# Kernel tuning notes

Measured on AMD Instinct MI355X. Metric: run time of the kernel, lower is better.

Reference implementation:

```python
import jax, jax.numpy as jnp
import numpy as np

HIDDEN = [256, 256, 256]
COND = 30
NB_STEPS = 20  # Clenshaw-Curtis quadrature order -> NB_STEPS+1 nodes


def cc_weights_steps(nb_steps):
    # Clenshaw-Curtis weights/nodes on [-1, 1] (UMNN compute_cc_weights)
    lam = np.arange(nb_steps + 1, dtype=np.float64).reshape(-1, 1)
    lam = np.cos(lam @ lam.T * np.pi / nb_steps)
    lam[:, 0] *= 0.5
    lam[:, -1] *= 0.5
    lam = lam * 2.0 / nb_steps
    W = np.arange(nb_steps + 1, dtype=np.float64).reshape(-1, 1)
    W[1::2] = 0.0
    W = 2.0 / (1.0 - W ** 2)
    W[0] = 1.0
    W[1::2] = 0.0
    cc_w = (lam.T @ W).flatten()          # [S]
    steps = np.cos(np.arange(nb_steps + 1) * np.pi / nb_steps)  # [S]
    return jnp.asarray(cc_w, jnp.float32), jnp.asarray(steps, jnp.float32)


def mlp(inp, Ws, bs):
    # IntegrandNet: Linear+ReLU chain, final layer ELU(x)+1 (strictly positive)
    y = inp
    n = len(Ws)
    for i in range(n):
        y = y @ Ws[i] + bs[i]
        y = jax.nn.relu(y) if i < n - 1 else jax.nn.elu(y) + 1.0
    return y[..., 0]


def setup_inputs() -> dict:
    key = jax.random.key(0)
    ks = jax.random.split(key, 12)
    B, D = 512, 32
    x = jax.random.normal(ks[0], (B, D), jnp.float32)
    h = jax.random.normal(ks[1], (B, D, COND), jnp.float32)
    dims = [1 + COND] + HIDDEN + [1]
    params = {}
    for i in range(len(dims) - 1):
        params[f"W{i}"] = jax.random.normal(ks[2 + 2 * i], (dims[i], dims[i + 1]), jnp.float32) / np.sqrt(dims[i]).astype(np.float32)
        params[f"b{i}"] = jnp.zeros((dims[i + 1],), jnp.float32)
    return {"x": x, "h": h, **params}


def reference(x, h, W0, b0, W1, b1, W2, b2, W3, b3):
    Ws = [W0, W1, W2, W3]
    bs = [b0, b1, b2, b3]
    B, D = x.shape
    S = NB_STEPS + 1
    cc_w, steps = cc_weights_steps(NB_STEPS)
    # x0 = 0, xT = x -> quadrature nodes X = xT * (steps + 1) / 2, shape [B, S, D]
    X = x[:, None, :] * (steps[None, :, None] + 1.0) * 0.5
    hb = jnp.broadcast_to(h[:, None, :, :], (B, S, D, COND))
    inp = jnp.concatenate([X[..., None], hb], axis=-1)  # [B, S, D, 1+COND]
    f = mlp(inp, Ws, bs)                                 # [B, S, D] positive integrand
    z_est = jnp.einsum('bsd,s->bd', f, cc_w) * x * 0.5   # integral over [0, x]
    z = z_est + h[:, :, 0]                               # add offset z0
    # second output: integrand evaluated at x (the transform's Jacobian diag)
    inp_x = jnp.concatenate([x[..., None], h], axis=-1)  # [B, D, 1+COND]
    jac = mlp(inp_x, Ws, bs)                             # [B, D]
    return z, jac
```

## Files before the change

kernel.cpp:

```cpp
#include <hip/hip_runtime.h>
#include <math.h>

#define NB        512
#define ND        32
#define NCOND     30
#define NS        21
#define NBD       (NB*ND)
#define BDPB      3
#define NBLK      ((NBD + BDPB - 1) / BDPB)

#define W0P_ELEMS (1*16*64*8)
#define W1P_ELEMS (8*16*64*8)
#define W3P_ELEMS (8*64*8)
#define WP_TOTAL  (W0P_ELEMS + 2*W1P_ELEMS + W3P_ELEMS)

typedef __bf16 bf8 __attribute__((ext_vector_type(8)));
typedef float  fx4 __attribute__((ext_vector_type(4)));
typedef unsigned short us8 __attribute__((ext_vector_type(8)));

__device__ __forceinline__ unsigned short f2bf(float f) {
  unsigned int u = __float_as_uint(f);
  u += 0x7FFFu + ((u >> 16) & 1u);
  return (unsigned short)(u >> 16);
}

__global__ void prep_pack(const float* __restrict__ W0,
                          const float* __restrict__ W1,
                          const float* __restrict__ W2,
                          const float* __restrict__ W3,
                          unsigned short* __restrict__ wp,
                          float* __restrict__ ccwbuf) {
  if (blockIdx.x == 0 && threadIdx.x < NS) {
    int tid = threadIdx.x;
    double acc = 0.0;
#pragma unroll
    for (int i = 0; i <= 20; i += 2) {
      double wi = (i == 0) ? 1.0 : 2.0 / (1.0 - (double)(i * i));
      acc += cos((double)(i * tid) * 3.141592653589793 / 20.0) * wi;
    }
    double edge = (tid == 0 || tid == 20) ? 0.5 : 1.0;
    ccwbuf[tid] = (float)(acc * 0.1 * edge);
  }
  int t = blockIdx.x * blockDim.x + threadIdx.x;
  if (t >= WP_TOTAL / 8) return;
  int base = t * 8;
  us8 out;
  if (base >= W0P_ELEMS + 2 * W1P_ELEMS) {
    int rem  = base - (W0P_ELEMS + 2 * W1P_ELEMS);
    int lane = (rem >> 3) & 63;
    int ktl  = rem >> 9;
    int k0   = ktl * 32 + (lane >> 4) * 8;
#pragma unroll
    for (int i = 0; i < 8; ++i)
      out[i] = ((lane & 15) == 0) ? f2bf(W3[k0 + i]) : (unsigned short)0;
  } else {
    const float* W; int rem, K;
    if (base < W0P_ELEMS)                  { W = W0; rem = base;                 K = 31;  }
    else if (base < W0P_ELEMS + W1P_ELEMS) { W = W1; rem = base - W0P_ELEMS;     K = 256; }
    else                                   { W = W2; rem = base - W0P_ELEMS - W1P_ELEMS; K = 256; }
    int lane = (rem >> 3) & 63;
    int ct   = (rem >> 9) & 15;
    int ktl  =  rem >> 13;
    int j  = ct * 16 + (lane & 15);
    int k0 = ktl * 32 + (lane >> 4) * 8;
#pragma unroll
    for (int i = 0; i < 8; ++i) {
      int k = k0 + i;
      out[i] = (k < K) ? f2bf(W[k * 256 + j]) : (unsigned short)0;
    }
  }
  *reinterpret_cast<us8*>(wp + base) = out;
}


#define ACC_BIAS(BIAS)                                                           \
  {                                                                              \
    float4 bq0 = *reinterpret_cast<const float4*>((BIAS) + (cgrp * 4 + 0) * 16 + khalf * 4); \
    float4 bq1 = *reinterpret_cast<const float4*>((BIAS) + (cgrp * 4 + 1) * 16 + khalf * 4); \
    float4 bq2 = *reinterpret_cast<const float4*>((BIAS) + (cgrp * 4 + 2) * 16 + khalf * 4); \
    float4 bq3 = *reinterpret_cast<const float4*>((BIAS) + (cgrp * 4 + 3) * 16 + khalf * 4); \
    _Pragma("unroll")                                                            \
    for (int rt = 0; rt < 4; ++rt) {                                             \
      acc[rt][0] = fx4{bq0.x, bq0.y, bq0.z, bq0.w};                              \
      acc[rt][1] = fx4{bq1.x, bq1.y, bq1.z, bq1.w};                              \
      acc[rt][2] = fx4{bq2.x, bq2.y, bq2.z, bq2.w};                              \
      acc[rt][3] = fx4{bq3.x, bq3.y, bq3.z, bq3.w};                              \
    }                                                                            \
  }

#define LOADW4(S0,S1,S2,S3, WB, KT)                                              \
  S0 = *reinterpret_cast<const bf8*>((WB) + (((KT) * 16 + cgrp * 4 + 0) * 64 + lane) * 8); \
  S1 = *reinterpret_cast<const bf8*>((WB) + (((KT) * 16 + cgrp * 4 + 1) * 64 + lane) * 8); \
  S2 = *reinterpret_cast<const bf8*>((WB) + (((KT) * 16 + cgrp * 4 + 2) * 64 + lane) * 8); \
  S3 = *reinterpret_cast<const bf8*>((WB) + (((KT) * 16 + cgrp * 4 + 3) * 64 + lane) * 8);

#define AOFF(M, KT) (((unsigned)((M) * 512 + (KT) * 64 + khalf * 16)) ^ ((unsigned)(((M) & 15) << 4)))

#define KSTEP(SRC, W0_,W1_,W2_,W3_, KT)                                          \
  {                                                                              \
    bf8 a0 = *reinterpret_cast<const bf8*>((SRC) + AOFF( 0 + colb, KT));         \
    bf8 a1 = *reinterpret_cast<const bf8*>((SRC) + AOFF(16 + colb, KT));         \
    bf8 a2 = *reinterpret_cast<const bf8*>((SRC) + AOFF(32 + colb, KT));         \
    bf8 a3 = *reinterpret_cast<const bf8*>((SRC) + AOFF(48 + colb, KT));         \
    __builtin_amdgcn_s_setprio(1);                                               \
    acc[0][0] = __builtin_amdgcn_mfma_f32_16x16x32_bf16(W0_, a0, acc[0][0], 0, 0, 0); \
    acc[0][1] = __builtin_amdgcn_mfma_f32_16x16x32_bf16(W1_, a0, acc[0][1], 0, 0, 0); \
    acc[0][2] = __builtin_amdgcn_mfma_f32_16x16x32_bf16(W2_, a0, acc[0][2], 0, 0, 0); \
    acc[0][3] = __builtin_amdgcn_mfma_f32_16x16x32_bf16(W3_, a0, acc[0][3], 0, 0, 0); \
    acc[1][0] = __builtin_amdgcn_mfma_f32_16x16x32_bf16(W0_, a1, acc[1][0], 0, 0, 0); \
    acc[1][1] = __builtin_amdgcn_mfma_f32_16x16x32_bf16(W1_, a1, acc[1][1], 0, 0, 0); \
    acc[1][2] = __builtin_amdgcn_mfma_f32_16x16x32_bf16(W2_, a1, acc[1][2], 0, 0, 0); \
    acc[1][3] = __builtin_amdgcn_mfma_f32_16x16x32_bf16(W3_, a1, acc[1][3], 0, 0, 0); \
    acc[2][0] = __builtin_amdgcn_mfma_f32_16x16x32_bf16(W0_, a2, acc[2][0], 0, 0, 0); \
    acc[2][1] = __builtin_amdgcn_mfma_f32_16x16x32_bf16(W1_, a2, acc[2][1], 0, 0, 0); \
    acc[2][2] = __builtin_amdgcn_mfma_f32_16x16x32_bf16(W2_, a2, acc[2][2], 0, 0, 0); \
    acc[2][3] = __builtin_amdgcn_mfma_f32_16x16x32_bf16(W3_, a2, acc[2][3], 0, 0, 0); \
    acc[3][0] = __builtin_amdgcn_mfma_f32_16x16x32_bf16(W0_, a3, acc[3][0], 0, 0, 0); \
    acc[3][1] = __builtin_amdgcn_mfma_f32_16x16x32_bf16(W1_, a3, acc[3][1], 0, 0, 0); \
    acc[3][2] = __builtin_amdgcn_mfma_f32_16x16x32_bf16(W2_, a3, acc[3][2], 0, 0, 0); \
    acc[3][3] = __builtin_amdgcn_mfma_f32_16x16x32_bf16(W3_, a3, acc[3][3], 0, 0, 0); \
    __builtin_amdgcn_s_setprio(0);                                               \
  }

#define DENSE_PIPE(SRC, WB, NWB)                                                 \
  KSTEP(SRC, wa0,wa1,wa2,wa3, 0) LOADW4(wa0,wa1,wa2,wa3, WB, 2)                  \
  KSTEP(SRC, wb0,wb1,wb2,wb3, 1) LOADW4(wb0,wb1,wb2,wb3, WB, 3)                  \
  KSTEP(SRC, wa0,wa1,wa2,wa3, 2) LOADW4(wa0,wa1,wa2,wa3, WB, 4)                  \
  KSTEP(SRC, wb0,wb1,wb2,wb3, 3) LOADW4(wb0,wb1,wb2,wb3, WB, 5)                  \
  KSTEP(SRC, wa0,wa1,wa2,wa3, 4) LOADW4(wa0,wa1,wa2,wa3, WB, 6)                  \
  KSTEP(SRC, wb0,wb1,wb2,wb3, 5) LOADW4(wb0,wb1,wb2,wb3, WB, 7)                  \
  KSTEP(SRC, wa0,wa1,wa2,wa3, 6) LOADW4(wa0,wa1,wa2,wa3, NWB, 0)                 \
  KSTEP(SRC, wb0,wb1,wb2,wb3, 7) LOADW4(wb0,wb1,wb2,wb3, NWB, 1)

#define DENSE_LAST(SRC, WB)                                                      \
  KSTEP(SRC, wa0,wa1,wa2,wa3, 0) LOADW4(wa0,wa1,wa2,wa3, WB, 2)                  \
  KSTEP(SRC, wb0,wb1,wb2,wb3, 1) LOADW4(wb0,wb1,wb2,wb3, WB, 3)                  \
  KSTEP(SRC, wa0,wa1,wa2,wa3, 2) LOADW4(wa0,wa1,wa2,wa3, WB, 4)                  \
  KSTEP(SRC, wb0,wb1,wb2,wb3, 3) LOADW4(wb0,wb1,wb2,wb3, WB, 5)                  \
  KSTEP(SRC, wa0,wa1,wa2,wa3, 4) LOADW4(wa0,wa1,wa2,wa3, WB, 6)                  \
  KSTEP(SRC, wb0,wb1,wb2,wb3, 5) LOADW4(wb0,wb1,wb2,wb3, WB, 7)                  \
  KSTEP(SRC, wa0,wa1,wa2,wa3, 6)                                                 \
  KSTEP(SRC, wb0,wb1,wb2,wb3, 7)

#define ACT_STORE(DST)                                                           \
  {                                                                              \
    _Pragma("unroll")                                                            \
    for (int rt = 0; rt < 4; ++rt) {                                             \
      int m = rt * 16 + colb;                                                    \
      unsigned int sbase = (unsigned int)(m * 512);                              \
      unsigned int swz   = (unsigned int)((m & 15) << 4);                        \
      _Pragma("unroll")                                                          \
      for (int ct = 0; ct < 4; ++ct) {                                           \
        int n0 = (cgrp * 4 + ct) * 16 + khalf * 4;                               \
        float v0 = fmaxf(acc[rt][ct][0], 0.f);                                   \
        float v1 = fmaxf(acc[rt][ct][1], 0.f);                                   \
        float v2 = fmaxf(acc[rt][ct][2], 0.f);                                   \
        float v3 = fmaxf(acc[rt][ct][3], 0.f);                                   \
        unsigned int p0, p1;                                                     \
        asm("v_cvt_pk_bf16_f32 %0, %1, %2" : "=v"(p0) : "v"(v0), "v"(v1));       \
        asm("v_cvt_pk_bf16_f32 %0, %1, %2" : "=v"(p1) : "v"(v2), "v"(v3));       \
        uint2 pk; pk.x = p0; pk.y = p1;                                          \
        *reinterpret_cast<uint2*>((DST) + ((sbase + (unsigned int)(n0 * 2)) ^ swz)) = pk; \
      }                                                                          \
    }                                                                            \
  }

__global__ __launch_bounds__(256, 2)
void mlp_kernel(const float* __restrict__ x, const float* __restrict__ h,
                const float* __restrict__ b0, const float* __restrict__ b1,
                const float* __restrict__ b2, const float* __restrict__ b3,
                const unsigned short* __restrict__ wp,
                const float* __restrict__ ccw,
                float* __restrict__ out) {
  __shared__ __align__(16) unsigned char ldsA[64 * 512];
  __shared__ __align__(16) unsigned char ldsB[64 * 512];
  __shared__ float ldsF[64];
  unsigned char* ldsIn = ldsB;

  int tid  = threadIdx.x;
  int wv   = tid >> 6;
  int lane = tid & 63;
  int cgrp = wv;
  int colb  = lane & 15;
  int khalf = lane >> 4;
  int blkbd = blockIdx.x * BDPB;

  const unsigned short* wb1p = wp + W0P_ELEMS;
  const unsigned short* wb2p = wp + W0P_ELEMS + W1P_ELEMS;
  const unsigned short* w3p  = wp + W0P_ELEMS + 2 * W1P_ELEMS;

  bf8 wa0, wa1, wa2, wa3, wb0, wb1, wb2, wb3;
  LOADW4(wa0, wa1, wa2, wa3, wp, 0);

  {
    int r = tid >> 2;
    int q = tid & 3;
    unsigned int u = (unsigned int)r / NS;
    int s = r - (int)u * NS;
    int bd = blkbd + (int)u;
    us8 au = us8{0,0,0,0,0,0,0,0};
    if (r < 63 && bd < NBD) {
      float xv = x[bd];
      float node = xv * (cosf((float)s * 0.15707963267948966f) + 1.0f) * 0.5f;
      const float* hrow = h + bd * NCOND;
#pragma unroll
      for (int i = 0; i < 8; ++i) {
        int c = q * 8 + i;
        float v;
        if (c == 0)       v = node;
        else if (c <= 30) v = hrow[c - 1];
        else              v = 0.0f;
        au[i] = f2bf(v);
      }
    }
    unsigned int off = (unsigned int)(r * 64 + q * 16) ^ (unsigned int)((r & 3) << 4);
    *reinterpret_cast<us8*>(ldsIn + off) = au;
  }
  __syncthreads();

  fx4 acc[4][4];

  {
    ACC_BIAS(b0);
#pragma unroll
    for (int rt = 0; rt < 4; ++rt) {
      int m = rt * 16 + colb;
      unsigned int off = (unsigned int)(m * 64 + khalf * 16) ^ (unsigned int)((m & 3) << 4);
      bf8 a = *reinterpret_cast<const bf8*>(ldsIn + off);
      acc[rt][0] = __builtin_amdgcn_mfma_f32_16x16x32_bf16(wa0, a, acc[rt][0], 0, 0, 0);
      acc[rt][1] = __builtin_amdgcn_mfma_f32_16x16x32_bf16(wa1, a, acc[rt][1], 0, 0, 0);
      acc[rt][2] = __builtin_amdgcn_mfma_f32_16x16x32_bf16(wa2, a, acc[rt][2], 0, 0, 0);
      acc[rt][3] = __builtin_amdgcn_mfma_f32_16x16x32_bf16(wa3, a, acc[rt][3], 0, 0, 0);
    }
    LOADW4(wa0, wa1, wa2, wa3, wb1p, 0);
    LOADW4(wb0, wb1, wb2, wb3, wb1p, 1);
    ACT_STORE(ldsA);
  }
  __syncthreads();

  ACC_BIAS(b1);
  DENSE_PIPE(ldsA, wb1p, wb2p);
  ACT_STORE(ldsB);
  __syncthreads();

  ACC_BIAS(b2);
  DENSE_LAST(ldsB, wb2p);
  ACT_STORE(ldsA);
  __syncthreads();

  {
    fx4 a3 = fx4{0.f, 0.f, 0.f, 0.f};
    int m = wv * 16 + colb;
    unsigned int abase = (unsigned int)(m * 512 + khalf * 16);
    unsigned int aswz  = (unsigned int)((m & 15) << 4);
#pragma unroll
    for (int kt = 0; kt < 8; ++kt) {
      bf8 w3f = *reinterpret_cast<const bf8*>(w3p + (kt * 64 + lane) * 8);
      bf8 a = *reinterpret_cast<const bf8*>(ldsA + ((abase + (unsigned)(kt * 64)) ^ aswz));
      a3 = __builtin_amdgcn_mfma_f32_16x16x32_bf16(w3f, a, a3, 0, 0, 0);
    }
    if (lane < 16) {
      float y = a3[0] + b3[0];
      float f = (y > 0.f) ? (y + 1.f) : expf(y);
      ldsF[wv * 16 + lane] = f;
    }
  }
  __syncthreads();

  if (tid < BDPB) {
    int bd = blkbd + tid;
    if (bd < NBD) {
      float acc2 = 0.f;
#pragma unroll
      for (int s2 = 0; s2 < NS; ++s2) acc2 += ldsF[tid * NS + s2] * ccw[s2];
      out[bd] = acc2 * x[bd] * 0.5f + h[bd * NCOND];
      out[NBD + bd] = ldsF[tid * NS];
    }
  }
}

extern "C" void kernel_launch(void* const* d_in, const int* in_sizes, int n_in,
                              void* d_out, int out_size, void* d_ws, size_t ws_size,
                              hipStream_t stream) {
  (void)in_sizes; (void)n_in; (void)out_size; (void)ws_size;
  const float* x  = (const float*)d_in[0];
  const float* h  = (const float*)d_in[1];
  const float* W0 = (const float*)d_in[2];
  const float* b0 = (const float*)d_in[3];
  const float* W1 = (const float*)d_in[4];
  const float* b1 = (const float*)d_in[5];
  const float* W2 = (const float*)d_in[6];
  const float* b2 = (const float*)d_in[7];
  const float* W3 = (const float*)d_in[8];
  const float* b3 = (const float*)d_in[9];

  unsigned short* wp = (unsigned short*)d_ws;
  float* ccwbuf = (float*)((char*)d_ws + WP_TOTAL * sizeof(unsigned short));
  float* out  = (float*)d_out;

  prep_pack<<<(WP_TOTAL / 8 + 255) / 256, 256, 0, stream>>>(W0, W1, W2, W3, wp, ccwbuf);
  mlp_kernel<<<NBLK, 256, 0, stream>>>(x, h, b0, b1, b2, b3, wp, ccwbuf, out);
}
```

Before: 101.0 us.

## Switch MLP GEMMs from 16x16x32 to 32x32x16 bf16 MFMA tiles

Repacks the weight layout and rewrites the dense-layer inner loops to use 32x32x16 MFMA instructions with four 32x32 accumulators per wave instead of sixteen 16x16 tiles. This cuts the number of MFMA issues and A-operand LDS reads per k-step, and restructures the final layer to run on two waves. Launch bounds drop from 2 to 1 block per CU, which frees registers but may reduce occupancy and latency hiding.

```diff
diff --git a/kernel.cpp b/kernel.cpp
--- a/kernel.cpp
+++ b/kernel.cpp
@@ -9,13 +9,13 @@
 #define BDPB      3
 #define NBLK      ((NBD + BDPB - 1) / BDPB)
 
-#define W0P_ELEMS (1*16*64*8)
-#define W1P_ELEMS (8*16*64*8)
-#define W3P_ELEMS (8*64*8)
+#define W0P_ELEMS (2*8*64*8)
+#define W1P_ELEMS (16*8*64*8)
+#define W3P_ELEMS (16*64*8)
 #define WP_TOTAL  (W0P_ELEMS + 2*W1P_ELEMS + W3P_ELEMS)
 
 typedef __bf16 bf8 __attribute__((ext_vector_type(8)));
-typedef float  fx4 __attribute__((ext_vector_type(4)));
+typedef float  fx16 __attribute__((ext_vector_type(16)));
 typedef unsigned short us8 __attribute__((ext_vector_type(8)));
 
 __device__ __forceinline__ unsigned short f2bf(float f) {
@@ -46,23 +46,23 @@
   int base = t * 8;
   us8 out;
   if (base >= W0P_ELEMS + 2 * W1P_ELEMS) {
-    int rem  = base - (W0P_ELEMS + 2 * W1P_ELEMS);
-    int lane = (rem >> 3) & 63;
-    int ktl  = rem >> 9;
-    int k0   = ktl * 32 + (lane >> 4) * 8;
+    int rem   = base - (W0P_ELEMS + 2 * W1P_ELEMS);
+    int lane  = (rem >> 3) & 63;
+    int kstep = rem >> 9;
+    int k0    = kstep * 16 + (lane >> 5) * 8;
 #pragma unroll
     for (int i = 0; i < 8; ++i)
-      out[i] = ((lane & 15) == 0) ? f2bf(W3[k0 + i]) : (unsigned short)0;
+      out[i] = ((lane & 31) == 0) ? f2bf(W3[k0 + i]) : (unsigned short)0;
   } else {
     const float* W; int rem, K;
     if (base < W0P_ELEMS)                  { W = W0; rem = base;                 K = 31;  }
     else if (base < W0P_ELEMS + W1P_ELEMS) { W = W1; rem = base - W0P_ELEMS;     K = 256; }
     else                                   { W = W2; rem = base - W0P_ELEMS - W1P_ELEMS; K = 256; }
-    int lane = (rem >> 3) & 63;
-    int ct   = (rem >> 9) & 15;
-    int ktl  =  rem >> 13;
-    int j  = ct * 16 + (lane & 15);
-    int k0 = ktl * 32 + (lane >> 4) * 8;
+    int lane  = (rem >> 3) & 63;
+    int ct    = (rem >> 9) & 7;
+    int kstep = rem >> 12;
+    int j  = ct * 32 + (lane & 31);
+    int k0 = kstep * 16 + (lane >> 5) * 8;
 #pragma unroll
     for (int i = 0; i < 8; ++i) {
       int k = k0 + i;
@@ -73,52 +73,29 @@
 }
 
 
-#define ACC_BIAS(BIAS)                                                           \
+#define AOFF32(M, KS) (((unsigned)((M) * 512 + (KS) * 32 + hi * 16)) ^ ((unsigned)(((M) & 15) << 4)))
+
+#define LOADW4(S0,S1,S2,S3, WB, KT)                                              \
+  S0 = *reinterpret_cast<const bf8*>((WB) + (((2*(KT)  ) * 8 + cgrp * 2 + 0) * 64 + lane) * 8); \
+  S1 = *reinterpret_cast<const bf8*>((WB) + (((2*(KT)  ) * 8 + cgrp * 2 + 1) * 64 + lane) * 8); \
+  S2 = *reinterpret_cast<const bf8*>((WB) + (((2*(KT)+1) * 8 + cgrp * 2 + 0) * 64 + lane) * 8); \
+  S3 = *reinterpret_cast<const bf8*>((WB) + (((2*(KT)+1) * 8 + cgrp * 2 + 1) * 64 + lane) * 8);
+
+#define KSTEP(SRC, W00,W01,W10,W11, KT)                                          \
   {                                                                              \
-    float4 bq0 = *reinterpret_cast<const float4*>((BIAS) + (cgrp * 4 + 0) * 16 + khalf * 4); \
-    float4 bq1 = *reinterpret_cast<const float4*>((BIAS) + (cgrp * 4 + 1) * 16 + khalf * 4); \
-    float4 bq2 = *reinterpret_cast<const float4*>((BIAS) + (cgrp * 4 + 2) * 16 + khalf * 4); \
-    float4 bq3 = *reinterpret_cast<const float4*>((BIAS) + (cgrp * 4 + 3) * 16 + khalf * 4); \
-    _Pragma("unroll")                                                            \
-    for (int rt = 0; rt < 4; ++rt) {                                             \
-      acc[rt][0] = fx4{bq0.x, bq0.y, bq0.z, bq0.w};                              \
-      acc[rt][1] = fx4{bq1.x, bq1.y, bq1.z, bq1.w};                              \
-      acc[rt][2] = fx4{bq2.x, bq2.y, bq2.z, bq2.w};                              \
-      acc[rt][3] = fx4{bq3.x, bq3.y, bq3.z, bq3.w};                              \
-    }                                                                            \
-  }
-
-#define LOADW4(S0,S1,S2,S3, WB, KT)                                              \
-  S0 = *reinterpret_cast<const bf8*>((WB) + (((KT) * 16 + cgrp * 4 + 0) * 64 + lane) * 8); \
-  S1 = *reinterpret_cast<const bf8*>((WB) + (((KT) * 16 + cgrp * 4 + 1) * 64 + lane) * 8); \
-  S2 = *reinterpret_cast<const bf8*>((WB) + (((KT) * 16 + cgrp * 4 + 2) * 64 + lane) * 8); \
-  S3 = *reinterpret_cast<const bf8*>((WB) + (((KT) * 16 + cgrp * 4 + 3) * 64 + lane) * 8);
-
-#define AOFF(M, KT) (((unsigned)((M) * 512 + (KT) * 64 + khalf * 16)) ^ ((unsigned)(((M) & 15) << 4)))
-
-#define KSTEP(SRC, W0_,W1_,W2_,W3_, KT)                                          \
-  {                                                                              \
-    bf8 a0 = *reinterpret_cast<const bf8*>((SRC) + AOFF( 0 + colb, KT));         \
-    bf8 a1 = *reinterpret_cast<const bf8*>((SRC) + AOFF(16 + colb, KT));         \
-    bf8 a2 = *reinterpret_cast<const bf8*>((SRC) + AOFF(32 + colb, KT));         \
-    bf8 a3 = *reinterpret_cast<const bf8*>((SRC) + AOFF(48 + colb, KT));         \
+    bf8 a00 = *reinterpret_cast<const bf8*>((SRC) + AOFF32(     l31, 2*(KT)  )); \
+    bf8 a10 = *reinterpret_cast<const bf8*>((SRC) + AOFF32(32 + l31, 2*(KT)  )); \
+    bf8 a01 = *reinterpret_cast<const bf8*>((SRC) + AOFF32(     l31, 2*(KT)+1)); \
+    bf8 a11 = *reinterpret_cast<const bf8*>((SRC) + AOFF32(32 + l31, 2*(KT)+1)); \
     __builtin_amdgcn_s_setprio(1);                                               \
-    acc[0][0] = __builtin_amdgcn_mfma_f32_16x16x32_bf16(W0_, a0, acc[0][0], 0, 0, 0); \
-    acc[0][1] = __builtin_amdgcn_mfma_f32_16x16x32_bf16(W1_, a0, acc[0][1], 0, 0, 0); \
-    acc[0][2] = __builtin_amdgcn_mfma_f32_16x16x32_bf16(W2_, a0, acc[0][2], 0, 0, 0); \
-    acc[0][3] = __builtin_amdgcn_mfma_f32_16x16x32_bf16(W3_, a0, acc[0][3], 0, 0, 0); \
-    acc[1][0] = __builtin_amdgcn_mfma_f32_16x16x32_bf16(W0_, a1, acc[1][0], 0, 0, 0); \
-    acc[1][1] = __builtin_amdgcn_mfma_f32_16x16x32_bf16(W1_, a1, acc[1][1], 0, 0, 0); \
-    acc[1][2] = __builtin_amdgcn_mfma_f32_16x16x32_bf16(W2_, a1, acc[1][2], 0, 0, 0); \
-    acc[1][3] = __builtin_amdgcn_mfma_f32_16x16x32_bf16(W3_, a1, acc[1][3], 0, 0, 0); \
-    acc[2][0] = __builtin_amdgcn_mfma_f32_16x16x32_bf16(W0_, a2, acc[2][0], 0, 0, 0); \
-    acc[2][1] = __builtin_amdgcn_mfma_f32_16x16x32_bf16(W1_, a2, acc[2][1], 0, 0, 0); \
-    acc[2][2] = __builtin_amdgcn_mfma_f32_16x16x32_bf16(W2_, a2, acc[2][2], 0, 0, 0); \
-    acc[2][3] = __builtin_amdgcn_mfma_f32_16x16x32_bf16(W3_, a2, acc[2][3], 0, 0, 0); \
-    acc[3][0] = __builtin_amdgcn_mfma_f32_16x16x32_bf16(W0_, a3, acc[3][0], 0, 0, 0); \
-    acc[3][1] = __builtin_amdgcn_mfma_f32_16x16x32_bf16(W1_, a3, acc[3][1], 0, 0, 0); \
-    acc[3][2] = __builtin_amdgcn_mfma_f32_16x16x32_bf16(W2_, a3, acc[3][2], 0, 0, 0); \
-    acc[3][3] = __builtin_amdgcn_mfma_f32_16x16x32_bf16(W3_, a3, acc[3][3], 0, 0, 0); \
+    cA = __builtin_amdgcn_mfma_f32_32x32x16_bf16(W00, a00, cA, 0, 0, 0);         \
+    cB = __builtin_amdgcn_mfma_f32_32x32x16_bf16(W01, a00, cB, 0, 0, 0);         \
+    cC = __builtin_amdgcn_mfma_f32_32x32x16_bf16(W00, a10, cC, 0, 0, 0);         \
+    cD = __builtin_amdgcn_mfma_f32_32x32x16_bf16(W01, a10, cD, 0, 0, 0);         \
+    cA = __builtin_amdgcn_mfma_f32_32x32x16_bf16(W10, a01, cA, 0, 0, 0);         \
+    cB = __builtin_amdgcn_mfma_f32_32x32x16_bf16(W11, a01, cB, 0, 0, 0);         \
+    cC = __builtin_amdgcn_mfma_f32_32x32x16_bf16(W10, a11, cC, 0, 0, 0);         \
+    cD = __builtin_amdgcn_mfma_f32_32x32x16_bf16(W11, a11, cD, 0, 0, 0);         \
     __builtin_amdgcn_s_setprio(0);                                               \
   }
 
@@ -142,30 +119,44 @@
   KSTEP(SRC, wa0,wa1,wa2,wa3, 6)                                                 \
   KSTEP(SRC, wb0,wb1,wb2,wb3, 7)
 
+#define ACC_BIAS1(ACC, BIAS, N0)                                                 \
+  {                                                                              \
+    float4 t0 = *reinterpret_cast<const float4*>((BIAS) + (N0) + 0 * 8 + hi * 4);\
+    float4 t1 = *reinterpret_cast<const float4*>((BIAS) + (N0) + 1 * 8 + hi * 4);\
+    float4 t2 = *reinterpret_cast<const float4*>((BIAS) + (N0) + 2 * 8 + hi * 4);\
+    float4 t3 = *reinterpret_cast<const float4*>((BIAS) + (N0) + 3 * 8 + hi * 4);\
+    ACC = fx16{t0.x,t0.y,t0.z,t0.w, t1.x,t1.y,t1.z,t1.w,                         \
+               t2.x,t2.y,t2.z,t2.w, t3.x,t3.y,t3.z,t3.w};                        \
+  }
+#define ACC_BIAS(BIAS)                                                           \
+  ACC_BIAS1(cA, BIAS, cgrp * 64 + 0)                                             \
+  ACC_BIAS1(cB, BIAS, cgrp * 64 + 32)                                            \
+  cC = cA; cD = cB;
+
+#define STORE1(DST, ACC, RT, CT)                                                 \
+  {                                                                              \
+    int m = (RT) * 32 + l31;                                                     \
+    unsigned int sbase = (unsigned int)(m * 512);                                \
+    unsigned int swz   = (unsigned int)((m & 15) << 4);                          \
+    _Pragma("unroll")                                                            \
+    for (int q = 0; q < 4; ++q) {                                                \
+      int n0 = cgrp * 64 + (CT) * 32 + q * 8 + hi * 4;                           \
+      float v0 = fmaxf(ACC[4*q+0], 0.f);                                         \
+      float v1 = fmaxf(ACC[4*q+1], 0.f);                                         \
+      float v2 = fmaxf(ACC[4*q+2], 0.f);                                         \
+      float v3 = fmaxf(ACC[4*q+3], 0.f);                                         \
+      unsigned int p0, p1;                                                       \
+      asm("v_cvt_pk_bf16_f32 %0, %1, %2" : "=v"(p0) : "v"(v0), "v"(v1));         \
+      asm("v_cvt_pk_bf16_f32 %0, %1, %2" : "=v"(p1) : "v"(v2), "v"(v3));         \
+      uint2 pk; pk.x = p0; pk.y = p1;                                            \
+      *reinterpret_cast<uint2*>((DST) + ((sbase + (unsigned int)(n0 * 2)) ^ swz)) = pk; \
+    }                                                                            \
+  }
 #define ACT_STORE(DST)                                                           \
-  {                                                                              \
-    _Pragma("unroll")                                                            \
-    for (int rt = 0; rt < 4; ++rt) {                                             \
-      int m = rt * 16 + colb;                                                    \
-      unsigned int sbase = (unsigned int)(m * 512);                              \
-      unsigned int swz   = (unsigned int)((m & 15) << 4);                        \
-      _Pragma("unroll")                                                          \
-      for (int ct = 0; ct < 4; ++ct) {                                           \
-        int n0 = (cgrp * 4 + ct) * 16 + khalf * 4;                               \
-        float v0 = fmaxf(acc[rt][ct][0], 0.f);                                   \
-        float v1 = fmaxf(acc[rt][ct][1], 0.f);                                   \
-        float v2 = fmaxf(acc[rt][ct][2], 0.f);                                   \
-        float v3 = fmaxf(acc[rt][ct][3], 0.f);                                   \
-        unsigned int p0, p1;                                                     \
-        asm("v_cvt_pk_bf16_f32 %0, %1, %2" : "=v"(p0) : "v"(v0), "v"(v1));       \
-        asm("v_cvt_pk_bf16_f32 %0, %1, %2" : "=v"(p1) : "v"(v2), "v"(v3));       \
-        uint2 pk; pk.x = p0; pk.y = p1;                                          \
-        *reinterpret_cast<uint2*>((DST) + ((sbase + (unsigned int)(n0 * 2)) ^ swz)) = pk; \
-      }                                                                          \
-    }                                                                            \
-  }
-
-__global__ __launch_bounds__(256, 2)
+  STORE1(DST, cA, 0, 0) STORE1(DST, cB, 0, 1)                                    \
+  STORE1(DST, cC, 1, 0) STORE1(DST, cD, 1, 1)
+
+__global__ __launch_bounds__(256, 1)
 void mlp_kernel(const float* __restrict__ x, const float* __restrict__ h,
                 const float* __restrict__ b0, const float* __restrict__ b1,
                 const float* __restrict__ b2, const float* __restrict__ b3,
@@ -181,8 +172,8 @@
   int wv   = tid >> 6;
   int lane = tid & 63;
   int cgrp = wv;
-  int colb  = lane & 15;
-  int khalf = lane >> 4;
+  int l31  = lane & 31;
+  int hi   = lane >> 5;
   int blkbd = blockIdx.x * BDPB;
 
   const unsigned short* wb1p = wp + W0P_ELEMS;
@@ -218,19 +209,31 @@
   }
   __syncthreads();
 
-  fx4 acc[4][4];
+  fx16 cA, cB, cC, cD;
 
   {
     ACC_BIAS(b0);
 #pragma unroll
-    for (int rt = 0; rt < 4; ++rt) {
-      int m = rt * 16 + colb;
-      unsigned int off = (unsigned int)(m * 64 + khalf * 16) ^ (unsigned int)((m & 3) << 4);
-      bf8 a = *reinterpret_cast<const bf8*>(ldsIn + off);
-      acc[rt][0] = __builtin_amdgcn_mfma_f32_16x16x32_bf16(wa0, a, acc[rt][0], 0, 0, 0);
-      acc[rt][1] = __builtin_amdgcn_mfma_f32_16x16x32_bf16(wa1, a, acc[rt][1], 0, 0, 0);
-      acc[rt][2] = __builtin_amdgcn_mfma_f32_16x16x32_bf16(wa2, a, acc[rt][2], 0, 0, 0);
-      acc[rt][3] = __builtin_amdgcn_mfma_f32_16x16x32_bf16(wa3, a, acc[rt][3], 0, 0, 0);
+    for (int ks = 0; ks < 2; ++ks) {
+      bf8 a0, a1;
+      {
+        int m0 = l31, m1 = 32 + l31;
+        unsigned int o0 = (unsigned int)(m0 * 64 + ks * 32 + hi * 16) ^ (unsigned int)((m0 & 3) << 4);
+        unsigned int o1 = (unsigned int)(m1 * 64 + ks * 32 + hi * 16) ^ (unsigned int)((m1 & 3) << 4);
+        a0 = *reinterpret_cast<const bf8*>(ldsIn + o0);
+        a1 = *reinterpret_cast<const bf8*>(ldsIn + o1);
+      }
+      if (ks == 0) {
+        cA = __builtin_amdgcn_mfma_f32_32x32x16_bf16(wa0, a0, cA, 0, 0, 0);
+        cB = __builtin_amdgcn_mfma_f32_32x32x16_bf16(wa1, a0, cB, 0, 0, 0);
+        cC = __builtin_amdgcn_mfma_f32_32x32x16_bf16(wa0, a1, cC, 0, 0, 0);
+        cD = __builtin_amdgcn_mfma_f32_32x32x16_bf16(wa1, a1, cD, 0, 0, 0);
+      } else {
+        cA = __builtin_amdgcn_mfma_f32_32x32x16_bf16(wa2, a0, cA, 0, 0, 0);
+        cB = __builtin_amdgcn_mfma_f32_32x32x16_bf16(wa3, a0, cB, 0, 0, 0);
+        cC = __builtin_amdgcn_mfma_f32_32x32x16_bf16(wa2, a1, cC, 0, 0, 0);
+        cD = __builtin_amdgcn_mfma_f32_32x32x16_bf16(wa3, a1, cD, 0, 0, 0);
+      }
     }
     LOADW4(wa0, wa1, wa2, wa3, wb1p, 0);
     LOADW4(wb0, wb1, wb2, wb3, wb1p, 1);
@@ -248,21 +251,19 @@
   ACT_STORE(ldsA);
   __syncthreads();
 
-  {
-    fx4 a3 = fx4{0.f, 0.f, 0.f, 0.f};
-    int m = wv * 16 + colb;
-    unsigned int abase = (unsigned int)(m * 512 + khalf * 16);
-    unsigned int aswz  = (unsigned int)((m & 15) << 4);
-#pragma unroll
-    for (int kt = 0; kt < 8; ++kt) {
-      bf8 w3f = *reinterpret_cast<const bf8*>(w3p + (kt * 64 + lane) * 8);
-      bf8 a = *reinterpret_cast<const bf8*>(ldsA + ((abase + (unsigned)(kt * 64)) ^ aswz));
-      a3 = __builtin_amdgcn_mfma_f32_16x16x32_bf16(w3f, a, a3, 0, 0, 0);
-    }
-    if (lane < 16) {
+  if (wv < 2) {
+    fx16 a3 = fx16{0.f,0.f,0.f,0.f, 0.f,0.f,0.f,0.f, 0.f,0.f,0.f,0.f, 0.f,0.f,0.f,0.f};
+    int m = wv * 32 + l31;
+#pragma unroll
+    for (int ks = 0; ks < 16; ++ks) {
+      bf8 w3f = *reinterpret_cast<const bf8*>(w3p + (ks * 64 + lane) * 8);
+      bf8 a = *reinterpret_cast<const bf8*>(ldsA + AOFF32(m, ks));
+      a3 = __builtin_amdgcn_mfma_f32_32x32x16_bf16(w3f, a, a3, 0, 0, 0);
+    }
+    if (lane < 32) {
       float y = a3[0] + b3[0];
       float f = (y > 0.f) ? (y + 1.f) : expf(y);
-      ldsF[wv * 16 + lane] = f;
+      ldsF[wv * 32 + lane] = f;
     }
   }
   __syncthreads();
```

Result: slower. 164.4 us (+62.7%).
